# Kernel optimization log

Measured on AMD Instinct MI355X. Metric: run time of the kernel, lower is better.

## Reference

```python
import jax, jax.numpy as jnp
import numpy as np

# Complete binary tree: B trees, L leaves each, processed level-synchronously.
B, L, IN_DIM, MEM = 64, 1024, 300, 256


def setup_inputs() -> dict:
    key = jax.random.key(0)
    ks = jax.random.split(key, 6)
    s = 0.05
    embs = jax.random.normal(ks[0], (B, L, IN_DIM), dtype=jnp.float32)
    # Leaf module: c = cx(x); h = sigmoid(ox(x)) * tanh(c)
    Wcx = jax.random.normal(ks[1], (MEM, IN_DIM), dtype=jnp.float32) * s
    bcx = jnp.zeros((MEM,), jnp.float32)
    Wox = jax.random.normal(ks[2], (MEM, IN_DIM), dtype=jnp.float32) * s
    box = jnp.zeros((MEM,), jnp.float32)
    # Composer: 4 gates (i, lf, rf, u), each gate = Linear(lh) + Linear(rh).
    # Stacked: Wl/Wr have shape [4, MEM, MEM]; biases [4, MEM].
    Wl = jax.random.normal(ks[3], (4, MEM, MEM), dtype=jnp.float32) * s
    bl = jnp.zeros((4, MEM), jnp.float32)
    Wr = jax.random.normal(ks[4], (4, MEM, MEM), dtype=jnp.float32) * s
    br = jnp.zeros((4, MEM), jnp.float32)
    return dict(embs=embs, Wcx=Wcx, bcx=bcx, Wox=Wox, box=box,
                Wl=Wl, bl=bl, Wr=Wr, br=br)


def reference(embs, Wcx, bcx, Wox, box, Wl, bl, Wr, br):
    # Leaf module (BinaryTreeLeafModule.forward), vectorized over all leaves.
    c = jnp.einsum('blx,mx->blm', embs, Wcx) + bcx          # [B, L, MEM]
    o = jax.nn.sigmoid(jnp.einsum('blx,mx->blm', embs, Wox) + box)
    h = o * jnp.tanh(c)

    bias = bl + br                                          # [4, MEM]
    n = c.shape[1]
    while n > 1:  # log2(L) levels, static unrolled loop
        lc, rc = c[:, 0::2], c[:, 1::2]                     # [B, n/2, MEM]
        lh, rh = h[:, 0::2], h[:, 1::2]
        # All 4 gate pre-activations fused: [B, n/2, 4, MEM]
        g = (jnp.einsum('bnm,gom->bngo', lh, Wl)
             + jnp.einsum('bnm,gom->bngo', rh, Wr) + bias)
        i = jax.nn.sigmoid(g[..., 0, :])
        lf = jax.nn.sigmoid(g[..., 1, :])
        rf = jax.nn.sigmoid(g[..., 2, :])
        u = jnp.tanh(g[..., 3, :])
        c = i * u + lf * lc + rf * rc                       # composer cell
        h = jnp.tanh(c)                                     # gate_output=False path
        n //= 2

    # Root state (tree.state = (c, h)); stacked as [2, B, MEM]
    return jnp.stack([c[:, 0], h[:, 0]])
```

## Files before the change

### kernel.cpp

```cpp
#include <hip/hip_runtime.h>
#include <hip/hip_bf16.h>


typedef __attribute__((ext_vector_type(8))) short bf16x8;
typedef __attribute__((ext_vector_type(4))) float f32x4;

__device__ __forceinline__ float fsig(float x)  { return 1.f / (1.f + __expf(-x)); }
__device__ __forceinline__ float ftanh(float x) { return 1.f - 2.f / (__expf(2.f * x) + 1.f); }
__device__ __forceinline__ ushort f2bf(float x) {
    __hip_bfloat16 b = __float2bfloat16(x);
    return *reinterpret_cast<ushort*>(&b);
}

__device__ __forceinline__ void gld_lds16(const void* g, void* l) {
    __builtin_amdgcn_global_load_lds((const __attribute__((address_space(1))) void*)g,
                                     (__attribute__((address_space(3))) void*)l, 16, 0, 0);
}

__global__ void conv_embs(const float* __restrict__ E, ushort* __restrict__ Eb)
{
    int tid = blockIdx.x * 256 + threadIdx.x;
    int row = tid / 80;
    int k = (tid - row * 80) * 4;
    float4 v = make_float4(0.f, 0.f, 0.f, 0.f);
    if (k < 300) v = *(const float4*)(E + (size_t)row * 300 + k);
    ushort4 o;
    o.x = f2bf(v.x); o.y = f2bf(v.y); o.z = f2bf(v.z); o.w = f2bf(v.w);
    *(ushort4*)(Eb + (size_t)row * 320 + k) = o;
}

__global__ void pack_leaf_k(const float* __restrict__ Wcx, const float* __restrict__ Wox,
                            const float* __restrict__ bcx, const float* __restrict__ box,
                            ushort* __restrict__ Wb, float* __restrict__ bp)
{
    int idx = blockIdx.x * 256 + threadIdx.x;
    if (idx < 163840) {
        int e = idx & 7, slot = (idx >> 3) & 3, o = (idx >> 5) & 255;
        int g = (idx >> 13) & 1, t = idx >> 14;
        int q = slot ^ (o & 3);
        int k = t * 32 + q * 8 + e;
        float v = 0.f;
        if (k < 300) v = g ? Wox[o * 300 + k] : Wcx[o * 300 + k];
        Wb[idx] = f2bf(v);
    }
    if (idx < 512) {
        int g = idx >> 8, o = idx & 255;
        bp[idx] = g ? box[o] : bcx[o];
    }
}

__global__ void pack_level_k(const float* __restrict__ Wl, const float* __restrict__ Wr,
                             const float* __restrict__ bl, const float* __restrict__ br,
                             ushort* __restrict__ Wb, float* __restrict__ bp)
{
    int idx = blockIdx.x * 256 + threadIdx.x;
    if (idx < 524288) {
        int e = idx & 7, slot = (idx >> 3) & 3, o = (idx >> 5) & 255;
        int g = (idx >> 13) & 3, t = idx >> 15;
        int q = slot ^ (o & 3);
        int k = t * 32 + q * 8 + e;
        float v = (k < 256) ? Wl[(g * 256 + o) * 256 + k]
                            : Wr[(g * 256 + o) * 256 + (k - 256)];
        Wb[idx] = f2bf(v);
    }
    if (idx < 1024) bp[idx] = bl[idx] + br[idx];
}


template<int NG, int NT, int MODE>
__global__ __launch_bounds__(256, 2)
void mfma_gemm(const ushort* __restrict__ A,
               const ushort* __restrict__ Wb,
               const float* __restrict__ bp,
               const float* __restrict__ Cprev,
               float* __restrict__ c_out,
               ushort* __restrict__ h_out,
               float* __restrict__ hf_out)
{
    constexpr int K = NT * 32;
    __shared__ __align__(16) ushort As[2][2048];
    __shared__ __align__(16) ushort Bs[2][NG * 2048];

    const int tid = threadIdx.x;
    const int wid = tid >> 6, ln = tid & 63;
    const int lq = ln >> 4, lr = ln & 15;
    const int wm = wid >> 1, wn = wid & 1;
    const int rowBlk = blockIdx.x * 64;
    const int o0 = blockIdx.y * 64;

    f32x4 acc[2][2][NG];
#pragma unroll
    for (int m = 0; m < 2; ++m)
#pragma unroll
        for (int n = 0; n < 2; ++n)
#pragma unroll
            for (int g = 0; g < NG; ++g) acc[m][n][g] = f32x4{0.f, 0.f, 0.f, 0.f};

    const int srow = wid * 16 + (ln >> 2);
    const int sq   = (ln & 3) ^ ((ln >> 2) & 3);
    const ushort* aRow = A + (size_t)(rowBlk + srow) * K + sq * 8;

    gld_lds16(aRow, &As[0][wid * 512]);
#pragma unroll
    for (int s = 0; s < NG; ++s)
        gld_lds16(Wb + ((size_t)s * 1024 + (o0 << 2) + wid * 64 + ln) * 8,
                  &Bs[0][(s * 256 + wid * 64) * 8]);

    for (int t = 0; t < NT; ++t) {
        __syncthreads();
        const int cur = t & 1;
        if (t + 1 < NT) {
            gld_lds16(aRow + (t + 1) * 32, &As[cur ^ 1][wid * 512]);
#pragma unroll
            for (int s = 0; s < NG; ++s)
                gld_lds16(Wb + ((size_t)((t + 1) * NG + s) * 1024 + (o0 << 2) + wid * 64 + ln) * 8,
                          &Bs[cur ^ 1][(s * 256 + wid * 64) * 8]);
        }
        bf16x8 a[2];
#pragma unroll
        for (int m = 0; m < 2; ++m) {
            int rL = wm * 32 + m * 16 + lr;
            a[m] = *(const bf16x8*)&As[cur][(rL * 4 + (lq ^ (lr & 3))) * 8];
        }
#pragma unroll
        for (int n = 0; n < 2; ++n) {
            int cL = wn * 32 + n * 16 + lr;
#pragma unroll
            for (int g = 0; g < NG; ++g) {
                bf16x8 b = *(const bf16x8*)&Bs[cur][((g * 64 + cL) * 4 + (lq ^ (lr & 3))) * 8];
#pragma unroll
                for (int m = 0; m < 2; ++m)
                    acc[m][n][g] = __builtin_amdgcn_mfma_f32_16x16x32_bf16(a[m], b, acc[m][n][g], 0, 0, 0);
            }
        }
    }

#pragma unroll
    for (int m = 0; m < 2; ++m)
#pragma unroll
    for (int n = 0; n < 2; ++n) {
        const int row0 = rowBlk + wm * 32 + m * 16 + lq * 4;
        const int col  = o0 + wn * 32 + n * 16 + lr;
        if constexpr (MODE == 0) {
            const float bc = bp[col], bo = bp[256 + col];
#pragma unroll
            for (int j = 0; j < 4; ++j) {
                int row = row0 + j;
                float cv = acc[m][n][0][j] + bc;
                float ov = acc[m][n][1][j] + bo;
                c_out[(size_t)row * 256 + col] = cv;
                h_out[(size_t)row * 256 + col] = f2bf(fsig(ov) * ftanh(cv));
            }
        } else {
            const float bi  = bp[col],       blf = bp[256 + col];
            const float brf = bp[512 + col], bu  = bp[768 + col];
#pragma unroll
            for (int j = 0; j < 4; ++j) {
                int row = row0 + j;
                float gi = fsig(acc[m][n][0][j] + bi);
                float lf = fsig(acc[m][n][1][j] + blf);
                float rf = fsig(acc[m][n][2][j] + brf);
                float gu = ftanh(acc[m][n][3][j] + bu);
                float lc = Cprev[(size_t)row * 512 + col];
                float rc = Cprev[(size_t)row * 512 + 256 + col];
                float cv = gi * gu + lf * lc + rf * rc;
                float hv = ftanh(cv);
                c_out[(size_t)row * 256 + col] = cv;
                if constexpr (MODE == 2) hf_out[(size_t)row * 256 + col] = hv;
                else                     h_out[(size_t)row * 256 + col] = f2bf(hv);
            }
        }
    }
}


extern "C" void kernel_launch(void* const* d_in, const int* in_sizes, int n_in,
                              void* d_out, int out_size, void* d_ws, size_t ws_size,
                              hipStream_t stream)
{
    const float* embs = (const float*)d_in[0];
    const float* Wcx  = (const float*)d_in[1];
    const float* bcx  = (const float*)d_in[2];
    const float* Wox  = (const float*)d_in[3];
    const float* box  = (const float*)d_in[4];
    const float* Wl   = (const float*)d_in[5];
    const float* bl   = (const float*)d_in[6];
    const float* Wr   = (const float*)d_in[7];
    const float* br   = (const float*)d_in[8];

    char* p = (char*)d_ws;
    ushort* Wb2 = (ushort*)p;  p += (size_t)524288 * 2;
    ushort* WbL = (ushort*)p;  p += (size_t)163840 * 2;
    float*  bp2 = (float*)p;   p += 1024 * 4;
    float*  bpL = (float*)p;   p += 512 * 4;
    float*  c0  = (float*)p;   p += (size_t)65536 * 256 * 4;
    ushort* h0  = (ushort*)p;  p += (size_t)65536 * 256 * 2;
    char* X = p;
    ushort* embsB = (ushort*)X;
    float*  cA = (float*)X;
    ushort* hA = (ushort*)(X + (size_t)32768 * 256 * 4);
    float*  cB = (float*)(X + (size_t)48 * 1024 * 1024);
    ushort* hB = (ushort*)(X + (size_t)64 * 1024 * 1024);

    conv_embs<<<20480, 256, 0, stream>>>(embs, embsB);
    pack_leaf_k<<<640, 256, 0, stream>>>(Wcx, Wox, bcx, box, WbL, bpL);
    pack_level_k<<<2048, 256, 0, stream>>>(Wl, Wr, bl, br, Wb2, bp2);

    mfma_gemm<2, 10, 0><<<dim3(1024, 4), 256, 0, stream>>>(
        embsB, WbL, bpL, nullptr, c0, h0, nullptr);

    const ushort* hin = h0;
    const float*  cin = c0;
    float*  cping[2] = {cA, cB};
    ushort* hping[2] = {hA, hB};
    int flip = 0;
    for (int np = 512; np >= 1; np >>= 1) {
        int M = 64 * np;
        if (np == 1) {
            mfma_gemm<4, 16, 2><<<dim3(1, 4), 256, 0, stream>>>(
                hin, Wb2, bp2, cin, (float*)d_out, nullptr, (float*)d_out + 64 * 256);
        } else {
            float* co = cping[flip]; ushort* ho = hping[flip];
            mfma_gemm<4, 16, 1><<<dim3(M / 64, 4), 256, 0, stream>>>(
                hin, Wb2, bp2, cin, co, ho, nullptr);
            cin = co; hin = ho; flip ^= 1;
        }
    }
}
```

Baseline: 283.7 us.

## Load A operand directly into registers and reassign waves to column strips

The A tile no longer goes through LDS. Each wave now loads all 64 rows of A straight from global memory into registers, with a one-step register prefetch, while the weights stay double-buffered in LDS. Wave tiling changes from a 2x2 split to each wave owning a 16-column strip across all 4 row blocks, and the LDS swizzle for the weights changes to (o>>1)&3 to match the new read pattern. Launch bounds go up to 3 blocks per SM. This removes LDS traffic and LDS space for A, but each wave now issues redundant uncoalesced global loads of A and needs more registers, which may conflict with the higher occupancy target.

```diff
diff --git a/kernel.cpp b/kernel.cpp
--- a/kernel.cpp
+++ b/kernel.cpp
@@ -37,7 +37,7 @@
     if (idx < 163840) {
         int e = idx & 7, slot = (idx >> 3) & 3, o = (idx >> 5) & 255;
         int g = (idx >> 13) & 1, t = idx >> 14;
-        int q = slot ^ (o & 3);
+        int q = slot ^ ((o >> 1) & 3);
         int k = t * 32 + q * 8 + e;
         float v = 0.f;
         if (k < 300) v = g ? Wox[o * 300 + k] : Wcx[o * 300 + k];
@@ -57,7 +57,7 @@
     if (idx < 524288) {
         int e = idx & 7, slot = (idx >> 3) & 3, o = (idx >> 5) & 255;
         int g = (idx >> 13) & 3, t = idx >> 15;
-        int q = slot ^ (o & 3);
+        int q = slot ^ ((o >> 1) & 3);
         int k = t * 32 + q * 8 + e;
         float v = (k < 256) ? Wl[(g * 256 + o) * 256 + k]
                             : Wr[(g * 256 + o) * 256 + (k - 256)];
@@ -68,7 +68,7 @@
 
 
 template<int NG, int NT, int MODE>
-__global__ __launch_bounds__(256, 2)
+__global__ __launch_bounds__(256, 3)
 void mfma_gemm(const ushort* __restrict__ A,
                const ushort* __restrict__ Wb,
                const float* __restrict__ bp,
@@ -78,89 +78,88 @@
                float* __restrict__ hf_out)
 {
     constexpr int K = NT * 32;
-    __shared__ __align__(16) ushort As[2][2048];
     __shared__ __align__(16) ushort Bs[2][NG * 2048];
 
     const int tid = threadIdx.x;
     const int wid = tid >> 6, ln = tid & 63;
     const int lq = ln >> 4, lr = ln & 15;
-    const int wm = wid >> 1, wn = wid & 1;
     const int rowBlk = blockIdx.x * 64;
     const int o0 = blockIdx.y * 64;
-
-    f32x4 acc[2][2][NG];
-#pragma unroll
-    for (int m = 0; m < 2; ++m)
-#pragma unroll
-        for (int n = 0; n < 2; ++n)
-#pragma unroll
-            for (int g = 0; g < NG; ++g) acc[m][n][g] = f32x4{0.f, 0.f, 0.f, 0.f};
-
-    const int srow = wid * 16 + (ln >> 2);
-    const int sq   = (ln & 3) ^ ((ln >> 2) & 3);
-    const ushort* aRow = A + (size_t)(rowBlk + srow) * K + sq * 8;
-
-    gld_lds16(aRow, &As[0][wid * 512]);
-#pragma unroll
-    for (int s = 0; s < NG; ++s)
-        gld_lds16(Wb + ((size_t)s * 1024 + (o0 << 2) + wid * 64 + ln) * 8,
-                  &Bs[0][(s * 256 + wid * 64) * 8]);
-
+    const int cL = wid * 16 + lr;
+    const int slotp = lq ^ ((lr >> 1) & 3);
+
+    f32x4 acc[4][NG];
+#pragma unroll
+    for (int m = 0; m < 4; ++m)
+#pragma unroll
+        for (int g = 0; g < NG; ++g) acc[m][g] = f32x4{0.f, 0.f, 0.f, 0.f};
+
+    const ushort* wsrc = Wb + (size_t)(o0 * 4 + wid * 64 + ln) * 8;
+    const ushort* aBase = A + (size_t)rowBlk * K + (size_t)lr * K + lq * 8;
+
+#pragma unroll
+    for (int j = 0; j < NG; ++j)
+        gld_lds16(wsrc + (size_t)j * 1024 * 8, &Bs[0][(j * 256 + wid * 64) * 8]);
+
+    bf16x8 a[4], an[4];
+#pragma unroll
+    for (int m = 0; m < 4; ++m)
+        a[m] = *(const bf16x8*)(aBase + (size_t)m * 16 * K);
+
+#pragma unroll
     for (int t = 0; t < NT; ++t) {
         __syncthreads();
         const int cur = t & 1;
         if (t + 1 < NT) {
-            gld_lds16(aRow + (t + 1) * 32, &As[cur ^ 1][wid * 512]);
-#pragma unroll
-            for (int s = 0; s < NG; ++s)
-                gld_lds16(Wb + ((size_t)((t + 1) * NG + s) * 1024 + (o0 << 2) + wid * 64 + ln) * 8,
-                          &Bs[cur ^ 1][(s * 256 + wid * 64) * 8]);
-        }
-        bf16x8 a[2];
-#pragma unroll
-        for (int m = 0; m < 2; ++m) {
-            int rL = wm * 32 + m * 16 + lr;
-            a[m] = *(const bf16x8*)&As[cur][(rL * 4 + (lq ^ (lr & 3))) * 8];
-        }
-#pragma unroll
-        for (int n = 0; n < 2; ++n) {
-            int cL = wn * 32 + n * 16 + lr;
-#pragma unroll
-            for (int g = 0; g < NG; ++g) {
-                bf16x8 b = *(const bf16x8*)&Bs[cur][((g * 64 + cL) * 4 + (lq ^ (lr & 3))) * 8];
-#pragma unroll
-                for (int m = 0; m < 2; ++m)
-                    acc[m][n][g] = __builtin_amdgcn_mfma_f32_16x16x32_bf16(a[m], b, acc[m][n][g], 0, 0, 0);
-            }
-        }
-    }
-
-#pragma unroll
-    for (int m = 0; m < 2; ++m)
-#pragma unroll
-    for (int n = 0; n < 2; ++n) {
-        const int row0 = rowBlk + wm * 32 + m * 16 + lq * 4;
-        const int col  = o0 + wn * 32 + n * 16 + lr;
-        if constexpr (MODE == 0) {
-            const float bc = bp[col], bo = bp[256 + col];
+#pragma unroll
+            for (int j = 0; j < NG; ++j)
+                gld_lds16(wsrc + (size_t)((t + 1) * NG + j) * 1024 * 8,
+                          &Bs[cur ^ 1][(j * 256 + wid * 64) * 8]);
+#pragma unroll
+            for (int m = 0; m < 4; ++m)
+                an[m] = *(const bf16x8*)(aBase + (size_t)m * 16 * K + (t + 1) * 32);
+        }
+#pragma unroll
+        for (int g = 0; g < NG; ++g) {
+            bf16x8 b = *(const bf16x8*)&Bs[cur][(g * 256 + cL * 4 + slotp) * 8];
+#pragma unroll
+            for (int m = 0; m < 4; ++m)
+                acc[m][g] = __builtin_amdgcn_mfma_f32_16x16x32_bf16(a[m], b, acc[m][g], 0, 0, 0);
+        }
+        if (t + 1 < NT) {
+#pragma unroll
+            for (int m = 0; m < 4; ++m) a[m] = an[m];
+        }
+    }
+
+    const int col = o0 + cL;
+    if constexpr (MODE == 0) {
+        const float bc = bp[col], bo = bp[256 + col];
+#pragma unroll
+        for (int m = 0; m < 4; ++m) {
+            const int row0 = rowBlk + m * 16 + lq * 4;
 #pragma unroll
             for (int j = 0; j < 4; ++j) {
                 int row = row0 + j;
-                float cv = acc[m][n][0][j] + bc;
-                float ov = acc[m][n][1][j] + bo;
+                float cv = acc[m][0][j] + bc;
+                float ov = acc[m][1][j] + bo;
                 c_out[(size_t)row * 256 + col] = cv;
                 h_out[(size_t)row * 256 + col] = f2bf(fsig(ov) * ftanh(cv));
             }
-        } else {
-            const float bi  = bp[col],       blf = bp[256 + col];
-            const float brf = bp[512 + col], bu  = bp[768 + col];
+        }
+    } else {
+        const float bi  = bp[col],       blf = bp[256 + col];
+        const float brf = bp[512 + col], bu  = bp[768 + col];
+#pragma unroll
+        for (int m = 0; m < 4; ++m) {
+            const int row0 = rowBlk + m * 16 + lq * 4;
 #pragma unroll
             for (int j = 0; j < 4; ++j) {
                 int row = row0 + j;
-                float gi = fsig(acc[m][n][0][j] + bi);
-                float lf = fsig(acc[m][n][1][j] + blf);
-                float rf = fsig(acc[m][n][2][j] + brf);
-                float gu = ftanh(acc[m][n][3][j] + bu);
+                float gi = fsig(acc[m][0][j] + bi);
+                float lf = fsig(acc[m][1][j] + blf);
+                float rf = fsig(acc[m][2][j] + brf);
+                float gu = ftanh(acc[m][3][j] + bu);
                 float lc = Cprev[(size_t)row * 512 + col];
                 float rc = Cprev[(size_t)row * 512 + 256 + col];
                 float cv = gi * gu + lf * lc + rf * rc;
@@ -215,13 +214,12 @@
     ushort* hping[2] = {hA, hB};
     int flip = 0;
     for (int np = 512; np >= 1; np >>= 1) {
-        int M = 64 * np;
         if (np == 1) {
             mfma_gemm<4, 16, 2><<<dim3(1, 4), 256, 0, stream>>>(
                 hin, Wb2, bp2, cin, (float*)d_out, nullptr, (float*)d_out + 64 * 256);
         } else {
             float* co = cping[flip]; ushort* ho = hping[flip];
-            mfma_gemm<4, 16, 1><<<dim3(M / 64, 4), 256, 0, stream>>>(
+            mfma_gemm<4, 16, 1><<<dim3(np, 4), 256, 0, stream>>>(
                 hin, Wb2, bp2, cin, co, ho, nullptr);
             cin = co; hin = ho; flip ^= 1;
         }
```

New measurement: 401.1 us. 41.4% more time.

## Enlarge GEMM block tile to 128 rows and widen leaf output tile

Applied to the files above, without the earlier changes.

Each block now computes a 128-row tile instead of 64 rows, so each wave holds 4 M-fragments and reuses every B fragment read from LDS across more MFMAs. The leaf GEMM also widens its output tile to 128 columns, giving a 512x2 grid. The LDS swizzle for both A and B is changed (including the weight packing kernels) to match the new layout. Row bounds checks handle the odd tail at the last levels. The risk is more accumulator registers and fewer blocks on small levels, which can cut occupancy and parallelism.

```diff
diff --git a/kernel.cpp b/kernel.cpp
--- a/kernel.cpp
+++ b/kernel.cpp
@@ -37,7 +37,7 @@
     if (idx < 163840) {
         int e = idx & 7, slot = (idx >> 3) & 3, o = (idx >> 5) & 255;
         int g = (idx >> 13) & 1, t = idx >> 14;
-        int q = slot ^ (o & 3);
+        int q = slot ^ ((o >> 1) & 3);
         int k = t * 32 + q * 8 + e;
         float v = 0.f;
         if (k < 300) v = g ? Wox[o * 300 + k] : Wcx[o * 300 + k];
@@ -57,7 +57,7 @@
     if (idx < 524288) {
         int e = idx & 7, slot = (idx >> 3) & 3, o = (idx >> 5) & 255;
         int g = (idx >> 13) & 3, t = idx >> 15;
-        int q = slot ^ (o & 3);
+        int q = slot ^ ((o >> 1) & 3);
         int k = t * 32 + q * 8 + e;
         float v = (k < 256) ? Wl[(g * 256 + o) * 256 + k]
                             : Wr[(g * 256 + o) * 256 + (k - 256)];
@@ -67,7 +67,7 @@
 }
 
 
-template<int NG, int NT, int MODE>
+template<int NG, int NT, int NO, int MODE>
 __global__ __launch_bounds__(256, 2)
 void mfma_gemm(const ushort* __restrict__ A,
                const ushort* __restrict__ Wb,
@@ -75,99 +75,117 @@
                const float* __restrict__ Cprev,
                float* __restrict__ c_out,
                ushort* __restrict__ h_out,
-               float* __restrict__ hf_out)
+               float* __restrict__ hf_out,
+               int M)
 {
     constexpr int K = NT * 32;
-    __shared__ __align__(16) ushort As[2][2048];
-    __shared__ __align__(16) ushort Bs[2][NG * 2048];
+    constexpr int NN = NO / 32;
+    __shared__ __align__(16) ushort As[2][512 * 8];
+    __shared__ __align__(16) ushort Bs[2][1024 * 8];
 
     const int tid = threadIdx.x;
     const int wid = tid >> 6, ln = tid & 63;
     const int lq = ln >> 4, lr = ln & 15;
     const int wm = wid >> 1, wn = wid & 1;
-    const int rowBlk = blockIdx.x * 64;
-    const int o0 = blockIdx.y * 64;
-
-    f32x4 acc[2][2][NG];
-#pragma unroll
-    for (int m = 0; m < 2; ++m)
-#pragma unroll
-        for (int n = 0; n < 2; ++n)
+    const int rowBlk = blockIdx.x * 128;
+    const int o0 = blockIdx.y * NO;
+
+    f32x4 acc[4][NN][NG];
+#pragma unroll
+    for (int m = 0; m < 4; ++m)
+#pragma unroll
+        for (int n = 0; n < NN; ++n)
 #pragma unroll
             for (int g = 0; g < NG; ++g) acc[m][n][g] = f32x4{0.f, 0.f, 0.f, 0.f};
 
-    const int srow = wid * 16 + (ln >> 2);
-    const int sq   = (ln & 3) ^ ((ln >> 2) & 3);
-    const ushort* aRow = A + (size_t)(rowBlk + srow) * K + sq * 8;
-
-    gld_lds16(aRow, &As[0][wid * 512]);
-#pragma unroll
-    for (int s = 0; s < NG; ++s)
-        gld_lds16(Wb + ((size_t)s * 1024 + (o0 << 2) + wid * 64 + ln) * 8,
+    const int aRow = wid * 16 + (ln >> 2);
+    const int aQ = ((ln & 3) - ((ln >> 3) & 3)) & 3;
+    const ushort* aSrc0 = A + (size_t)(rowBlk + aRow) * K + aQ * 8;
+    const ushort* aSrc1 = A + (size_t)(rowBlk + 64 + aRow) * K + aQ * 8;
+
+    const int aSw = (lq + ((lr >> 1) & 3)) & 3;
+    const int bSw = lq ^ ((lr >> 1) & 3);
+
+
+    gld_lds16(aSrc0, &As[0][(wid * 64) * 8]);
+    gld_lds16(aSrc1, &As[0][(256 + wid * 64) * 8]);
+#pragma unroll
+    for (int s = 0; s < 4; ++s) {
+        const int cL = s * 256 + wid * 64 + ln;
+        const int g = cL / (NO * 4), w = cL & (NO * 4 - 1);
+        gld_lds16(Wb + ((size_t)g * 1024 + o0 * 4 + w) * 8,
                   &Bs[0][(s * 256 + wid * 64) * 8]);
-
+    }
+
+#pragma unroll
     for (int t = 0; t < NT; ++t) {
         __syncthreads();
         const int cur = t & 1;
         if (t + 1 < NT) {
-            gld_lds16(aRow + (t + 1) * 32, &As[cur ^ 1][wid * 512]);
-#pragma unroll
-            for (int s = 0; s < NG; ++s)
-                gld_lds16(Wb + ((size_t)((t + 1) * NG + s) * 1024 + (o0 << 2) + wid * 64 + ln) * 8,
+            gld_lds16(aSrc0 + (t + 1) * 32, &As[cur ^ 1][(wid * 64) * 8]);
+            gld_lds16(aSrc1 + (t + 1) * 32, &As[cur ^ 1][(256 + wid * 64) * 8]);
+#pragma unroll
+            for (int s = 0; s < 4; ++s) {
+                const int cL = s * 256 + wid * 64 + ln;
+                const int g = cL / (NO * 4), w = cL & (NO * 4 - 1);
+                gld_lds16(Wb + ((size_t)((t + 1) * NG + g) * 1024 + o0 * 4 + w) * 8,
                           &Bs[cur ^ 1][(s * 256 + wid * 64) * 8]);
+            }
         }
-        bf16x8 a[2];
-#pragma unroll
-        for (int m = 0; m < 2; ++m) {
-            int rL = wm * 32 + m * 16 + lr;
-            a[m] = *(const bf16x8*)&As[cur][(rL * 4 + (lq ^ (lr & 3))) * 8];
-        }
-#pragma unroll
-        for (int n = 0; n < 2; ++n) {
-            int cL = wn * 32 + n * 16 + lr;
+        bf16x8 a[4];
+#pragma unroll
+        for (int m = 0; m < 4; ++m)
+            a[m] = *(const bf16x8*)&As[cur][((wm * 64 + m * 16 + lr) * 4 + aSw) * 8];
+#pragma unroll
+        for (int n = 0; n < NN; ++n)
 #pragma unroll
             for (int g = 0; g < NG; ++g) {
-                bf16x8 b = *(const bf16x8*)&Bs[cur][((g * 64 + cL) * 4 + (lq ^ (lr & 3))) * 8];
-#pragma unroll
-                for (int m = 0; m < 2; ++m)
+                bf16x8 b = *(const bf16x8*)
+                    &Bs[cur][(g * (NO * 4) + (wn * (NO / 2) + n * 16 + lr) * 4 + bSw) * 8];
+#pragma unroll
+                for (int m = 0; m < 4; ++m)
                     acc[m][n][g] = __builtin_amdgcn_mfma_f32_16x16x32_bf16(a[m], b, acc[m][n][g], 0, 0, 0);
             }
-        }
-    }
-
-#pragma unroll
-    for (int m = 0; m < 2; ++m)
-#pragma unroll
-    for (int n = 0; n < 2; ++n) {
-        const int row0 = rowBlk + wm * 32 + m * 16 + lq * 4;
-        const int col  = o0 + wn * 32 + n * 16 + lr;
-        if constexpr (MODE == 0) {
-            const float bc = bp[col], bo = bp[256 + col];
-#pragma unroll
-            for (int j = 0; j < 4; ++j) {
-                int row = row0 + j;
-                float cv = acc[m][n][0][j] + bc;
-                float ov = acc[m][n][1][j] + bo;
-                c_out[(size_t)row * 256 + col] = cv;
-                h_out[(size_t)row * 256 + col] = f2bf(fsig(ov) * ftanh(cv));
-            }
-        } else {
-            const float bi  = bp[col],       blf = bp[256 + col];
-            const float brf = bp[512 + col], bu  = bp[768 + col];
-#pragma unroll
-            for (int j = 0; j < 4; ++j) {
-                int row = row0 + j;
-                float gi = fsig(acc[m][n][0][j] + bi);
-                float lf = fsig(acc[m][n][1][j] + blf);
-                float rf = fsig(acc[m][n][2][j] + brf);
-                float gu = ftanh(acc[m][n][3][j] + bu);
-                float lc = Cprev[(size_t)row * 512 + col];
-                float rc = Cprev[(size_t)row * 512 + 256 + col];
-                float cv = gi * gu + lf * lc + rf * rc;
-                float hv = ftanh(cv);
-                c_out[(size_t)row * 256 + col] = cv;
-                if constexpr (MODE == 2) hf_out[(size_t)row * 256 + col] = hv;
-                else                     h_out[(size_t)row * 256 + col] = f2bf(hv);
+    }
+
+#pragma unroll
+    for (int m = 0; m < 4; ++m) {
+        const int row0 = rowBlk + wm * 64 + m * 16 + lq * 4;
+#pragma unroll
+        for (int n = 0; n < NN; ++n) {
+            const int col = o0 + wn * (NO / 2) + n * 16 + lr;
+            if constexpr (MODE == 0) {
+                const float bc = bp[col], bo = bp[256 + col];
+#pragma unroll
+                for (int j = 0; j < 4; ++j) {
+                    int row = row0 + j;
+                    if (row < M) {
+                        float cv = acc[m][n][0][j] + bc;
+                        float ov = acc[m][n][1][j] + bo;
+                        c_out[(size_t)row * 256 + col] = cv;
+                        h_out[(size_t)row * 256 + col] = f2bf(fsig(ov) * ftanh(cv));
+                    }
+                }
+            } else {
+                const float bi  = bp[col],       blf = bp[256 + col];
+                const float brf = bp[512 + col], bu  = bp[768 + col];
+#pragma unroll
+                for (int j = 0; j < 4; ++j) {
+                    int row = row0 + j;
+                    if (row < M) {
+                        float gi = fsig(acc[m][n][0][j] + bi);
+                        float lf = fsig(acc[m][n][1][j] + blf);
+                        float rf = fsig(acc[m][n][2][j] + brf);
+                        float gu = ftanh(acc[m][n][3][j] + bu);
+                        float lc = Cprev[(size_t)row * 512 + col];
+                        float rc = Cprev[(size_t)row * 512 + 256 + col];
+                        float cv = gi * gu + lf * lc + rf * rc;
+                        float hv = ftanh(cv);
+                        c_out[(size_t)row * 256 + col] = cv;
+                        if constexpr (MODE == 2) hf_out[(size_t)row * 256 + col] = hv;
+                        else                     h_out[(size_t)row * 256 + col] = f2bf(hv);
+                    }
+                }
             }
         }
     }
@@ -206,8 +224,8 @@
     pack_leaf_k<<<640, 256, 0, stream>>>(Wcx, Wox, bcx, box, WbL, bpL);
     pack_level_k<<<2048, 256, 0, stream>>>(Wl, Wr, bl, br, Wb2, bp2);
 
-    mfma_gemm<2, 10, 0><<<dim3(1024, 4), 256, 0, stream>>>(
-        embsB, WbL, bpL, nullptr, c0, h0, nullptr);
+    mfma_gemm<2, 10, 128, 0><<<dim3(512, 2), 256, 0, stream>>>(
+        embsB, WbL, bpL, nullptr, c0, h0, nullptr, 65536);
 
     const ushort* hin = h0;
     const float*  cin = c0;
@@ -215,14 +233,13 @@
     ushort* hping[2] = {hA, hB};
     int flip = 0;
     for (int np = 512; np >= 1; np >>= 1) {
-        int M = 64 * np;
         if (np == 1) {
-            mfma_gemm<4, 16, 2><<<dim3(1, 4), 256, 0, stream>>>(
-                hin, Wb2, bp2, cin, (float*)d_out, nullptr, (float*)d_out + 64 * 256);
+            mfma_gemm<4, 16, 64, 2><<<dim3(1, 4), 256, 0, stream>>>(
+                hin, Wb2, bp2, cin, (float*)d_out, nullptr, (float*)d_out + 64 * 256, 64);
         } else {
             float* co = cping[flip]; ushort* ho = hping[flip];
-            mfma_gemm<4, 16, 1><<<dim3(M / 64, 4), 256, 0, stream>>>(
-                hin, Wb2, bp2, cin, co, ho, nullptr);
+            mfma_gemm<4, 16, 64, 1><<<dim3((np + 1) / 2, 4), 256, 0, stream>>>(
+                hin, Wb2, bp2, cin, co, ho, nullptr, 64 * np);
             cin = co; hin = ho; flip ^= 1;
         }
     }
```

Result: slower. 367.3 us (+29.5%).
